# Optimization experiments

Hardware: AMD Instinct MI355X
Metric: run time of the kernel (lower is better)

The kernel has to match this reference:

```python
import jax, jax.numpy as jnp
import numpy as np

NEG = -1e9  # finite stand-in for -inf so downstream grads stay finite
NUM_HEADS = 16


def phm_linear(x, A, S, b):
    # PHM weight: W = sum_i kron(A[i], S[i]) -> (n*kin, n*kout)
    n, kin, kout = S.shape
    W = jnp.einsum('nab,nkl->akbl', A, S).reshape(n * kin, n * kout)
    return x @ W + b


def layer_norm(x, g, b, eps=1e-5):
    mu = jnp.mean(x, axis=-1, keepdims=True)
    var = jnp.var(x, axis=-1, keepdims=True)
    return (x - mu) / jnp.sqrt(var + eps) * g + b


def masking(V, lens):
    # DAG transition mask: vertex i may transition to j>i with j < len[b].
    i = jnp.arange(V)
    tri = i[None, :] > i[:, None]                       # (V,V) j > i
    valid = i[None, None, :] < lens[:, None, None]      # (B,1,V)
    m = tri[None, :, :] & valid
    dead = ~m.any(-1)                                   # (B,V) rows with no valid successor
    eye = jnp.eye(V, dtype=bool)
    m = m | (dead[:, :, None] & eye[None])              # keep softmax finite on dead rows
    return m, dead


def setup_inputs() -> dict:
    key = jax.random.key(0)
    ks = jax.random.split(key, 8)
    B, V, E, VOC = 8, 512, 1024, 32000
    s = 0.02
    return {
        'x': jax.random.normal(ks[0], (B, V, E), jnp.float32),
        'vertex_lens': jax.random.randint(ks[1], (B,), V // 2, V + 1),
        'ln_g': jnp.ones((E,), jnp.float32),
        'ln_b': jnp.zeros((E,), jnp.float32),
        'attn_A': jax.random.normal(ks[2], (4, 4, 4), jnp.float32) * 0.5,
        'attn_S': jax.random.normal(ks[3], (4, 256, 512), jnp.float32) * s,
        'attn_b': jnp.zeros((2 * E,), jnp.float32),
        'gate_A': jax.random.normal(ks[4], (4, 4, 4), jnp.float32) * 0.5,
        'gate_S': jax.random.normal(ks[5], (4, 256, 4), jnp.float32) * s,
        'gate_b': jnp.zeros((NUM_HEADS,), jnp.float32),
        'lm_A': jax.random.normal(ks[6], (2, 2, 2), jnp.float32) * 0.5,
        'lm_S': jax.random.normal(ks[7], (2, 512, 16000), jnp.float32) * s,
        'lm_b': jnp.zeros((VOC,), jnp.float32),
    }


def reference(x, vertex_lens, ln_g, ln_b, attn_A, attn_S, attn_b,
              gate_A, gate_S, gate_b, lm_A, lm_S, lm_b):
    B, V, E = x.shape
    H = NUM_HEADS
    cs = E // H
    xn = layer_norm(x, ln_g, ln_b)
    m, r = masking(V, vertex_lens)
    # gate over heads (B,V,H)
    g = jax.nn.log_softmax(phm_linear(xn, gate_A, gate_S, gate_b), axis=-1)
    qk = phm_linear(xn, attn_A, attn_S, attn_b)
    q, k = jnp.split(qk, 2, axis=-1)
    q = q.reshape(B, V, H, cs)
    k = k.reshape(B, V, H, cs)
    scores = jnp.einsum('bihf,bjhf->bijh', q, k) / jnp.asarray(np.sqrt(cs), jnp.float32)
    scores = jnp.where(m[..., None], scores, NEG)
    scores = jax.nn.log_softmax(scores, axis=2)          # normalize over successors j
    scores = jnp.where(r[:, :, None, None], NEG, scores)  # kill rows past length
    transition_matrix = jax.nn.logsumexp(scores + g[:, :, None, :], axis=-1)  # (B,V,V)
    vocab_log_probs = jax.nn.log_softmax(phm_linear(xn, lm_A, lm_S, lm_b), axis=-1)
    return transition_matrix, vocab_log_probs
```

## Files before the change

### kernel.cpp

```cpp
#include <hip/hip_runtime.h>
#include <hip/hip_bf16.h>
#include <stdint.h>

typedef __bf16 bf16x8 __attribute__((ext_vector_type(8)));
typedef __bf16 bf16x4 __attribute__((ext_vector_type(4)));
typedef float  f32x4  __attribute__((ext_vector_type(4)));

typedef __attribute__((address_space(3))) unsigned int as3_uint;
typedef const __attribute__((address_space(1))) unsigned int as1_uint;

#define NEGC (-1e9f)

__device__ __forceinline__ void async16(void* ldsPtr, const void* gPtr) {
    __builtin_amdgcn_global_load_lds((as1_uint*)(uintptr_t)gPtr,
                                     (as3_uint*)(uintptr_t)ldsPtr, 16, 0, 0);
}

__global__ __launch_bounds__(256) void ln_kernel(const float* __restrict__ x,
                                                 const float* __restrict__ gw,
                                                 const float* __restrict__ bw,
                                                 __bf16* __restrict__ xn) {
    __shared__ float red[8];
    size_t row = blockIdx.x;
    int t = threadIdx.x;
    const float4* xr = (const float4*)(x + row * 1024);
    float4 v = xr[t];
    float s  = v.x + v.y + v.z + v.w;
    float ss = v.x*v.x + v.y*v.y + v.z*v.z + v.w*v.w;
    #pragma unroll
    for (int o = 32; o; o >>= 1) { s += __shfl_xor(s, o); ss += __shfl_xor(ss, o); }
    int wave = t >> 6, lane = t & 63;
    if (lane == 0) { red[wave*2] = s; red[wave*2+1] = ss; }
    __syncthreads();
    float S  = red[0] + red[2] + red[4] + red[6];
    float SS = red[1] + red[3] + red[5] + red[7];
    float mu  = S * (1.0f/1024.0f);
    float var = SS * (1.0f/1024.0f) - mu*mu;
    float rs  = rsqrtf(var + 1e-5f);
    float4 gv = ((const float4*)gw)[t];
    float4 bv = ((const float4*)bw)[t];
    bf16x4 o4;
    o4[0] = (__bf16)((v.x-mu)*rs*gv.x + bv.x);
    o4[1] = (__bf16)((v.y-mu)*rs*gv.y + bv.y);
    o4[2] = (__bf16)((v.z-mu)*rs*gv.z + bv.z);
    o4[3] = (__bf16)((v.w-mu)*rs*gv.w + bv.w);
    ((bf16x4*)(xn + row*1024))[t] = o4;
}

__global__ __launch_bounds__(256) void phm_build(const float* __restrict__ A,
                                                 const float* __restrict__ S,
                                                 __bf16* __restrict__ Wt,
                                                 int nn, int kin, int kout) {
    __shared__ float sh[4][32][65];
    __shared__ float shA[64];
    int t  = threadIdx.x;
    int l0 = blockIdx.x * 64;
    int k0 = blockIdx.y * 32;
    int kt = nn * kin;
    if (t < nn*nn*nn) shA[t] = A[t];
    for (int n = 0; n < nn; ++n) {
        #pragma unroll
        for (int i = 0; i < 8; ++i) {
            int e = t + i*256;
            int kk = e >> 6, ll = e & 63;
            sh[n][kk][ll] = S[((size_t)(n*kin) + k0 + kk)*kout + l0 + ll];
        }
    }
    __syncthreads();
    for (int a = 0; a < nn; ++a)
        for (int b = 0; b < nn; ++b) {
            #pragma unroll
            for (int i = 0; i < 8; ++i) {
                int e = t + i*256;
                int kk = e & 31, ll = e >> 5;
                float val = 0.f;
                for (int n = 0; n < nn; ++n)
                    val += shA[(n*nn + a)*nn + b] * sh[n][kk][ll];
                Wt[(size_t)(b*kout + l0 + ll)*kt + a*kin + k0 + kk] = (__bf16)val;
            }
        }
}

__global__ __launch_bounds__(256) void gatew_kernel(const float* __restrict__ A,
                                                    const float* __restrict__ S,
                                                    float* __restrict__ W) {
    int idx = blockIdx.x*256 + threadIdx.x;
    int r = idx >> 4, c = idx & 15;
    int a = r >> 8, k = r & 255, b = c >> 2, l = c & 3;
    float v = 0.f;
    #pragma unroll
    for (int n = 0; n < 4; ++n)
        v += A[(n*4 + a)*4 + b] * S[((size_t)(n*256 + k))*4 + l];
    W[idx] = v;
}

template<int SWZ, int BF16OUT>
__global__ __launch_bounds__(256) void gemm_bt_t(const __bf16* __restrict__ A,
                                                 const __bf16* __restrict__ Bt,
                                                 const float* __restrict__ bias,
                                                 void* __restrict__ Cv,
                                                 int M, int N, int K) {
    __shared__ __align__(16) __bf16 As[128*64];
    __shared__ __align__(16) __bf16 Bs[128*64];
    int tid  = threadIdx.x;
    int wave = tid >> 6, lane = tid & 63;
    int m0, n0;
    if (SWZ) {
        int bid  = blockIdx.x;
        int wg   = (bid & 7) * 1000 + (bid >> 3);
        int band = wg / 2000;
        int rem  = wg % 2000;
        int nt   = rem >> 3;
        int mt   = band * 8 + (rem & 7);
        m0 = mt * 128; n0 = nt * 128;
    } else {
        m0 = blockIdx.y * 128; n0 = blockIdx.x * 128;
    }
    int wm = (wave >> 1) * 64, wn = (wave & 1) * 64;
    int lrow = lane & 15, lk = lane >> 4;
    f32x4 acc[4][4] = {};
    for (int k0 = 0; k0 < K; k0 += 64) {
        #pragma unroll
        for (int q = 0; q < 4; ++q) {
            int o   = q*4096 + tid*16;
            int row = o >> 7;
            int sp  = (o >> 4) & 7;
            int s   = sp ^ (row & 7);
            async16((char*)As + q*4096 + wave*1024,
                    (const char*)A  + ((size_t)(m0+row)*K + k0 + s*8)*2);
            async16((char*)Bs + q*4096 + wave*1024,
                    (const char*)Bt + ((size_t)(n0+row)*K + k0 + s*8)*2);
        }
        __syncthreads();
        #pragma unroll
        for (int kk = 0; kk < 2; ++kk) {
            bf16x8 af[4], bfr[4];
            #pragma unroll
            for (int mi = 0; mi < 4; ++mi) {
                int r = wm + mi*16 + lrow;
                int off = r*128 + ((kk*64 + lk*16) ^ ((r & 7) << 4));
                af[mi] = *(const bf16x8*)((const char*)As + off);
            }
            #pragma unroll
            for (int ni = 0; ni < 4; ++ni) {
                int r = wn + ni*16 + lrow;
                int off = r*128 + ((kk*64 + lk*16) ^ ((r & 7) << 4));
                bfr[ni] = *(const bf16x8*)((const char*)Bs + off);
            }
            #pragma unroll
            for (int mi = 0; mi < 4; ++mi)
                #pragma unroll
                for (int ni = 0; ni < 4; ++ni)
                    acc[mi][ni] = __builtin_amdgcn_mfma_f32_16x16x32_bf16(
                        af[mi], bfr[ni], acc[mi][ni], 0, 0, 0);
        }
        __syncthreads();
    }
    #pragma unroll
    for (int ni = 0; ni < 4; ++ni) {
        int col = n0 + wn + ni*16 + lrow;
        float bv = bias ? bias[col] : 0.f;
        #pragma unroll
        for (int mi = 0; mi < 4; ++mi) {
            #pragma unroll
            for (int r = 0; r < 4; ++r) {
                int rowg = m0 + wm + mi*16 + lk*4 + r;
                float val = acc[mi][ni][r] + bv;
                if (BF16OUT) {
                    __bf16* rowp = (__bf16*)((char*)Cv + (size_t)rowg*N*4);
                    rowp[col] = (__bf16)val;
                } else {
                    ((float*)Cv)[(size_t)rowg*N + col] = val;
                }
            }
        }
    }
}

__global__ __launch_bounds__(256) void gate_kernel(const __bf16* __restrict__ xn,
                                                   const float* __restrict__ Wg,
                                                   const float* __restrict__ gb,
                                                   float* __restrict__ Gp) {
    __shared__ float xr[16][65];
    __shared__ float red[16][17];
    size_t row = blockIdx.x;
    int t = threadIdx.x;
    bf16x4 v = ((const bf16x4*)(xn + row*1024))[t];
    #pragma unroll
    for (int q = 0; q < 4; ++q) {
        int e = t*4 + q;
        xr[e >> 6][e & 63] = (float)v[q];
    }
    __syncthreads();
    int h = t & 15, sl = t >> 4;
    float p = 0.f;
    #pragma unroll
    for (int u = 0; u < 64; ++u) p += xr[sl][u] * Wg[(sl*64 + u)*16 + h];
    red[sl][h] = p;
    __syncthreads();
    if (t < 16) {
        float logit = gb[t];
        #pragma unroll
        for (int s2 = 0; s2 < 16; ++s2) logit += red[s2][t];
        float m = logit;
        #pragma unroll
        for (int o = 8; o; o >>= 1) m = fmaxf(m, __shfl_xor(m, o, 16));
        float e = __expf(logit - m);
        float ssum = e;
        #pragma unroll
        for (int o = 8; o; o >>= 1) ssum += __shfl_xor(ssum, o, 16);
        Gp[row*16 + t] = e / ssum;
    }
}

__global__ __launch_bounds__(256) void scores_kernel(const float* __restrict__ qk,
                                                     const float* __restrict__ Gp,
                                                     const int* __restrict__ lens,
                                                     float* __restrict__ out) {
    __shared__ float qs[8][1024];
    __shared__ float gps[8][16];
    __shared__ float wredB[2][4][8];
    int bid = blockIdx.x;
    int b   = bid & 7;
    int i0  = (bid >> 3) * 8;
    int t   = threadIdx.x;
    int wave = t >> 6, lane = t & 63;
    int len = lens[b];
    const float4* qbase = (const float4*)(qk + ((size_t)b*512 + i0)*2048);
    #pragma unroll
    for (int s = 0; s < 8; ++s) {
        int e = t + s*256;
        int ti = e >> 8, c4 = e & 255;
        ((float4*)qs)[e] = qbase[ti*512 + c4];
    }
    if (t < 128) gps[t >> 4][t & 15] = Gp[((size_t)b*512 + i0 + (t >> 4))*16 + (t & 15)];
    __syncthreads();
    int j0 = t, j1 = t + 256;
    const float4* kp0 = (const float4*)(qk + ((size_t)b*512 + j0)*2048 + 1024);
    const float4* kp1 = (const float4*)(qk + ((size_t)b*512 + j1)*2048 + 1024);
    float acc0[8] = {}, acc1[8] = {}, mace[8] = {};
    for (int h = 0; h < 16; ++h) {
        float4 kv0[16], kv1[16];
        #pragma unroll
        for (int u = 0; u < 16; ++u) { kv0[u] = kp0[h*16 + u]; kv1[u] = kp1[h*16 + u]; }
        float pex0[8], pex1[8];
        #pragma unroll
        for (int ti = 0; ti < 8; ++ti) {
            const float* qrow = &qs[ti][h*64];
            float d0 = 0.f, d1 = 0.f;
            #pragma unroll
            for (int u = 0; u < 16; ++u) {
                float q0 = qrow[u*4+0], q1 = qrow[u*4+1], q2 = qrow[u*4+2], q3 = qrow[u*4+3];
                d0 += kv0[u].x*q0 + kv0[u].y*q1 + kv0[u].z*q2 + kv0[u].w*q3;
                d1 += kv1[u].x*q0 + kv1[u].y*q1 + kv1[u].z*q2 + kv1[u].w*q3;
            }
            int i = i0 + ti;
            float sc0 = (j0 > i && j0 < len) ? d0 * 0.125f : NEGC;
            float sc1 = (j1 > i && j1 < len) ? d1 * 0.125f : NEGC;
            float pe0 = __expf(sc0), pe1 = __expf(sc1);
            pex0[ti] = pe0; pex1[ti] = pe1;
            float vv = pe0 + pe1;
            #pragma unroll
            for (int o = 32; o; o >>= 1) vv += __shfl_xor(vv, o);
            if (lane == 0) wredB[h & 1][wave][ti] = vv;
        }
        __syncthreads();
        #pragma unroll
        for (int ti = 0; ti < 8; ++ti) {
            float gs = wredB[h & 1][0][ti] + wredB[h & 1][1][ti]
                     + wredB[h & 1][2][ti] + wredB[h & 1][3][ti];
            float inv = 1.0f / gs;
            float g = gps[ti][h];
            acc0[ti] += pex0[ti] * inv * g;
            acc1[ti] += pex1[ti] * inv * g;
            mace[ti] += g * inv;
        }
    }
    #pragma unroll
    for (int ti = 0; ti < 8; ++ti) {
        int i = i0 + ti;
        float lm = NEGC + __logf(mace[ti]);
        float v0, v1;
        if (i >= len - 1) { v0 = NEGC; v1 = NEGC; }
        else {
            v0 = (j0 > i && j0 < len) ? __logf(acc0[ti]) : lm;
            v1 = (j1 > i && j1 < len) ? __logf(acc1[ti]) : lm;
        }
        out[((size_t)b*512 + i)*512 + j0] = v0;
        out[((size_t)b*512 + i)*512 + j1] = v1;
    }
}

__global__ __launch_bounds__(256) void vocab_softmax_bf16(float* __restrict__ out) {
    __shared__ __align__(16) __bf16 srow[32000];
    __shared__ float red[8];
    size_t row = blockIdx.x;
    char* rowbase = (char*)out + row * (size_t)32000 * 4;
    const bf16x8* g8 = (const bf16x8*)rowbase;
    bf16x8* s8 = (bf16x8*)srow;
    int t = threadIdx.x, wave = t >> 6, lane = t & 63;
    float mx = -1e30f;
    for (int v = t; v < 4000; v += 256) {
        bf16x8 c = g8[v];
        s8[v] = c;
        #pragma unroll
        for (int jj = 0; jj < 8; ++jj) mx = fmaxf(mx, (float)c[jj]);
    }
    #pragma unroll
    for (int o = 32; o; o >>= 1) mx = fmaxf(mx, __shfl_xor(mx, o));
    if (lane == 0) red[wave] = mx;
    __syncthreads();
    mx = fmaxf(fmaxf(red[0], red[1]), fmaxf(red[2], red[3]));
    float sum = 0.f;
    for (int v = t; v < 4000; v += 256) {
        bf16x8 c = s8[v];
        #pragma unroll
        for (int jj = 0; jj < 8; ++jj) sum += __expf((float)c[jj] - mx);
    }
    #pragma unroll
    for (int o = 32; o; o >>= 1) sum += __shfl_xor(sum, o);
    if (lane == 0) red[4 + wave] = sum;
    __syncthreads();
    float lse = mx + __logf(red[4] + red[5] + red[6] + red[7]);
    float4* o4 = (float4*)rowbase;
    for (int u = t; u < 8000; u += 256) {
        bf16x4 c = *(const bf16x4*)(srow + u*4);
        float4 a;
        a.x = (float)c[0] - lse; a.y = (float)c[1] - lse;
        a.z = (float)c[2] - lse; a.w = (float)c[3] - lse;
        o4[u] = a;
    }
}

extern "C" void kernel_launch(void* const* d_in, const int* in_sizes, int n_in,
                              void* d_out, int out_size, void* d_ws, size_t ws_size,
                              hipStream_t stream) {
    (void)in_sizes; (void)n_in; (void)out_size; (void)ws_size;
    const float* x      = (const float*)d_in[0];
    const int*   lens   = (const int*)  d_in[1];
    const float* ln_g   = (const float*)d_in[2];
    const float* ln_b   = (const float*)d_in[3];
    const float* attn_A = (const float*)d_in[4];
    const float* attn_S = (const float*)d_in[5];
    const float* attn_b = (const float*)d_in[6];
    const float* gate_A = (const float*)d_in[7];
    const float* gate_S = (const float*)d_in[8];
    const float* gate_b = (const float*)d_in[9];
    const float* lm_A   = (const float*)d_in[10];
    const float* lm_S   = (const float*)d_in[11];
    const float* lm_b   = (const float*)d_in[12];

    float* out_trans = (float*)d_out;
    float* out_vocab = out_trans + (size_t)8*512*512;

    char* ws = (char*)d_ws;
    __bf16* xn     = (__bf16*)(ws);
    __bf16* WtAttn = (__bf16*)(ws + 8388608);
    __bf16* WtLm   = (__bf16*)(ws + 12582912);
    float*  Wg     = (float*) (ws + 78118912);
    float*  qkbuf  = (float*) (ws + 78184448);
    float*  Gp     = (float*) (ws + 111738880);

    hipLaunchKernelGGL(ln_kernel,    dim3(4096),     dim3(256), 0, stream, x, ln_g, ln_b, xn);
    hipLaunchKernelGGL(gatew_kernel, dim3(64),       dim3(256), 0, stream, gate_A, gate_S, Wg);
    hipLaunchKernelGGL(phm_build,    dim3(8, 8),     dim3(256), 0, stream, attn_A, attn_S, WtAttn, 4, 256, 512);
    hipLaunchKernelGGL(phm_build,    dim3(250, 16),  dim3(256), 0, stream, lm_A, lm_S, WtLm, 2, 512, 16000);
    hipLaunchKernelGGL((gemm_bt_t<0,0>), dim3(16, 32), dim3(256), 0, stream,
                       xn, WtAttn, attn_b, (void*)qkbuf, 4096, 2048, 1024);
    hipLaunchKernelGGL(gate_kernel,  dim3(4096),     dim3(256), 0, stream, xn, Wg, gate_b, Gp);
    hipLaunchKernelGGL(scores_kernel,dim3(512),      dim3(256), 0, stream, qkbuf, Gp, lens, out_trans);
    hipLaunchKernelGGL((gemm_bt_t<1,1>), dim3(8000),  dim3(256), 0, stream,
                       xn, WtLm, lm_b, (void*)out_vocab, 4096, 32000, 1024);
    hipLaunchKernelGGL(vocab_softmax_bf16, dim3(4096), dim3(256), 0, stream, out_vocab);
}
```

Baseline: 837.3 us.

## Run LM-head GEMM in FP8 e4m3 with MFMA scale instructions

LayerNorm now also writes an FP8 e4m3 copy of the normalized activations, and the LM PHM weight is built directly in FP8, pre-scaled by 16 to keep small weights out of the subnormal range. A new GEMM kernel uses the 16x16x128 f8f6f4 scaled MFMA with K-tiles of 128 and undoes the scale in the epilogue. The goal is to halve operand bandwidth and raise matrix throughput for the largest GEMM, at the cost of much lower precision in the vocab logits. The attention GEMM stays in bf16 and the workspace layout is reorganized.

```diff
diff --git a/kernel.cpp b/kernel.cpp
--- a/kernel.cpp
+++ b/kernel.cpp
@@ -1,10 +1,13 @@
 #include <hip/hip_runtime.h>
 #include <hip/hip_bf16.h>
+#include <hip/hip_fp8.h>
 #include <stdint.h>
 
 typedef __bf16 bf16x8 __attribute__((ext_vector_type(8)));
 typedef __bf16 bf16x4 __attribute__((ext_vector_type(4)));
 typedef float  f32x4  __attribute__((ext_vector_type(4)));
+typedef int    i32x4  __attribute__((ext_vector_type(4)));
+typedef int    i32x8  __attribute__((ext_vector_type(8)));
 
 typedef __attribute__((address_space(3))) unsigned int as3_uint;
 typedef const __attribute__((address_space(1))) unsigned int as1_uint;
@@ -19,7 +22,8 @@
 __global__ __launch_bounds__(256) void ln_kernel(const float* __restrict__ x,
                                                  const float* __restrict__ gw,
                                                  const float* __restrict__ bw,
-                                                 __bf16* __restrict__ xn) {
+                                                 __bf16* __restrict__ xn,
+                                                 unsigned char* __restrict__ xn8) {
     __shared__ float red[8];
     size_t row = blockIdx.x;
     int t = threadIdx.x;
@@ -39,17 +43,24 @@
     float rs  = rsqrtf(var + 1e-5f);
     float4 gv = ((const float4*)gw)[t];
     float4 bv = ((const float4*)bw)[t];
+    float f0 = (v.x-mu)*rs*gv.x + bv.x;
+    float f1 = (v.y-mu)*rs*gv.y + bv.y;
+    float f2 = (v.z-mu)*rs*gv.z + bv.z;
+    float f3 = (v.w-mu)*rs*gv.w + bv.w;
     bf16x4 o4;
-    o4[0] = (__bf16)((v.x-mu)*rs*gv.x + bv.x);
-    o4[1] = (__bf16)((v.y-mu)*rs*gv.y + bv.y);
-    o4[2] = (__bf16)((v.z-mu)*rs*gv.z + bv.z);
-    o4[3] = (__bf16)((v.w-mu)*rs*gv.w + bv.w);
+    o4[0] = (__bf16)f0; o4[1] = (__bf16)f1; o4[2] = (__bf16)f2; o4[3] = (__bf16)f3;
     ((bf16x4*)(xn + row*1024))[t] = o4;
-}
-
+    unsigned int pk = (unsigned)__hip_fp8_e4m3(f0).__x
+                    | ((unsigned)__hip_fp8_e4m3(f1).__x << 8)
+                    | ((unsigned)__hip_fp8_e4m3(f2).__x << 16)
+                    | ((unsigned)__hip_fp8_e4m3(f3).__x << 24);
+    ((unsigned int*)(xn8 + row*1024))[t] = pk;
+}
+
+template<int OUT>
 __global__ __launch_bounds__(256) void phm_build(const float* __restrict__ A,
                                                  const float* __restrict__ S,
-                                                 __bf16* __restrict__ Wt,
+                                                 void* __restrict__ Wt,
                                                  int nn, int kin, int kout) {
     __shared__ float sh[4][32][65];
     __shared__ float shA[64];
@@ -76,7 +87,9 @@
                 float val = 0.f;
                 for (int n = 0; n < nn; ++n)
                     val += shA[(n*nn + a)*nn + b] * sh[n][kk][ll];
-                Wt[(size_t)(b*kout + l0 + ll)*kt + a*kin + k0 + kk] = (__bf16)val;
+                size_t idx = (size_t)(b*kout + l0 + ll)*kt + a*kin + k0 + kk;
+                if (OUT == 0) ((__bf16*)Wt)[idx] = (__bf16)val;
+                else          ((unsigned char*)Wt)[idx] = __hip_fp8_e4m3(val * 16.0f).__x;
             }
         }
 }
@@ -94,28 +107,16 @@
     W[idx] = v;
 }
 
-template<int SWZ, int BF16OUT>
-__global__ __launch_bounds__(256) void gemm_bt_t(const __bf16* __restrict__ A,
-                                                 const __bf16* __restrict__ Bt,
-                                                 const float* __restrict__ bias,
-                                                 void* __restrict__ Cv,
-                                                 int M, int N, int K) {
+__global__ __launch_bounds__(256) void gemm_bt(const __bf16* __restrict__ A,
+                                               const __bf16* __restrict__ Bt,
+                                               const float* __restrict__ bias,
+                                               float* __restrict__ C,
+                                               int M, int N, int K) {
     __shared__ __align__(16) __bf16 As[128*64];
     __shared__ __align__(16) __bf16 Bs[128*64];
     int tid  = threadIdx.x;
     int wave = tid >> 6, lane = tid & 63;
-    int m0, n0;
-    if (SWZ) {
-        int bid  = blockIdx.x;
-        int wg   = (bid & 7) * 1000 + (bid >> 3);
-        int band = wg / 2000;
-        int rem  = wg % 2000;
-        int nt   = rem >> 3;
-        int mt   = band * 8 + (rem & 7);
-        m0 = mt * 128; n0 = nt * 128;
-    } else {
-        m0 = blockIdx.y * 128; n0 = blockIdx.x * 128;
-    }
+    int m0 = blockIdx.y * 128, n0 = blockIdx.x * 128;
     int wm = (wave >> 1) * 64, wn = (wave & 1) * 64;
     int lrow = lane & 15, lk = lane >> 4;
     f32x4 acc[4][4] = {};
@@ -165,13 +166,81 @@
             #pragma unroll
             for (int r = 0; r < 4; ++r) {
                 int rowg = m0 + wm + mi*16 + lk*4 + r;
-                float val = acc[mi][ni][r] + bv;
-                if (BF16OUT) {
-                    __bf16* rowp = (__bf16*)((char*)Cv + (size_t)rowg*N*4);
-                    rowp[col] = (__bf16)val;
-                } else {
-                    ((float*)Cv)[(size_t)rowg*N + col] = val;
-                }
+                C[(size_t)rowg*N + col] = acc[mi][ni][r] + bv;
+            }
+        }
+    }
+}
+
+__global__ __launch_bounds__(256) void gemm_mx_lm(const unsigned char* __restrict__ A8,
+                                                  const unsigned char* __restrict__ B8,
+                                                  const float* __restrict__ bias,
+                                                  void* __restrict__ Cv) {
+    const int K = 1024, N = 32000;
+    __shared__ __align__(16) unsigned char As[128*128];
+    __shared__ __align__(16) unsigned char Bs[128*128];
+    int tid = threadIdx.x;
+    int wave = tid >> 6, lane = tid & 63;
+    int bid  = blockIdx.x;
+    int wg   = (bid & 7) * 1000 + (bid >> 3);
+    int band = wg / 2000;
+    int rem  = wg % 2000;
+    int nt   = rem >> 3;
+    int mt   = band * 8 + (rem & 7);
+    int m0 = mt * 128, n0 = nt * 128;
+    int wm = (wave >> 1) * 64, wn = (wave & 1) * 64;
+    int lrow = lane & 15, lk = lane >> 4;
+    f32x4 acc[4][4] = {};
+    for (int k0 = 0; k0 < K; k0 += 128) {
+        #pragma unroll
+        for (int q = 0; q < 4; ++q) {
+            int o = q*4096 + tid*16;
+            int r = o >> 7;
+            int p = (o >> 4) & 7;
+            int g = p ^ (r & 7);
+            async16((char*)As + q*4096 + wave*1024,
+                    (const char*)A8 + (size_t)(m0+r)*K + k0 + g*16);
+            async16((char*)Bs + q*4096 + wave*1024,
+                    (const char*)B8 + (size_t)(n0+r)*K + k0 + g*16);
+        }
+        __syncthreads();
+        i32x8 af[4], bfr[4];
+        #pragma unroll
+        for (int mi = 0; mi < 4; ++mi) {
+            int r = wm + mi*16 + lrow;
+            int c0 = lk*2;
+            i32x4 lo = *(const i32x4*)(As + r*128 + ((c0    ^ (r&7))*16));
+            i32x4 hi = *(const i32x4*)(As + r*128 + (((c0+1) ^ (r&7))*16));
+            af[mi] = __builtin_shufflevector(lo, hi, 0,1,2,3,4,5,6,7);
+        }
+        #pragma unroll
+        for (int ni = 0; ni < 4; ++ni) {
+            int r = wn + ni*16 + lrow;
+            int c0 = lk*2;
+            i32x4 lo = *(const i32x4*)(Bs + r*128 + ((c0    ^ (r&7))*16));
+            i32x4 hi = *(const i32x4*)(Bs + r*128 + (((c0+1) ^ (r&7))*16));
+            bfr[ni] = __builtin_shufflevector(lo, hi, 0,1,2,3,4,5,6,7);
+        }
+        #pragma unroll
+        for (int mi = 0; mi < 4; ++mi)
+            #pragma unroll
+            for (int ni = 0; ni < 4; ++ni)
+                acc[mi][ni] = __builtin_amdgcn_mfma_scale_f32_16x16x128_f8f6f4(
+                    af[mi], bfr[ni], acc[mi][ni],
+                    0 , 0 , 0, 127, 0, 127);
+        __syncthreads();
+    }
+    #pragma unroll
+    for (int ni = 0; ni < 4; ++ni) {
+        int col = n0 + wn + ni*16 + lrow;
+        float bv = bias ? bias[col] : 0.f;
+        #pragma unroll
+        for (int mi = 0; mi < 4; ++mi) {
+            #pragma unroll
+            for (int r = 0; r < 4; ++r) {
+                int rowg = m0 + wm + mi*16 + lk*4 + r;
+                float val = acc[mi][ni][r] * 0.0625f + bv;
+                ((__bf16*)((char*)Cv + (size_t)rowg * N * 4))[col] = (__bf16)val;
             }
         }
     }
@@ -354,22 +423,23 @@
     float* out_vocab = out_trans + (size_t)8*512*512;
 
     char* ws = (char*)d_ws;
-    __bf16* xn     = (__bf16*)(ws);
-    __bf16* WtAttn = (__bf16*)(ws + 8388608);
-    __bf16* WtLm   = (__bf16*)(ws + 12582912);
-    float*  Wg     = (float*) (ws + 78118912);
-    float*  qkbuf  = (float*) (ws + 78184448);
-    float*  Gp     = (float*) (ws + 111738880);
-
-    hipLaunchKernelGGL(ln_kernel,    dim3(4096),     dim3(256), 0, stream, x, ln_g, ln_b, xn);
+    __bf16*        xn     = (__bf16*)(ws);
+    unsigned char* xn8    = (unsigned char*)(ws + 8388608);
+    __bf16*        WtAttn = (__bf16*)(ws + 12582912);
+    unsigned char* WtLm8  = (unsigned char*)(ws + 16777216);
+    float*         Wg     = (float*)(ws + 49545216);
+    float*         qkbuf  = (float*)(ws + 49610752);
+    float*         Gp     = (float*)(ws + 83165184);
+
+    hipLaunchKernelGGL(ln_kernel,    dim3(4096),     dim3(256), 0, stream, x, ln_g, ln_b, xn, xn8);
     hipLaunchKernelGGL(gatew_kernel, dim3(64),       dim3(256), 0, stream, gate_A, gate_S, Wg);
-    hipLaunchKernelGGL(phm_build,    dim3(8, 8),     dim3(256), 0, stream, attn_A, attn_S, WtAttn, 4, 256, 512);
-    hipLaunchKernelGGL(phm_build,    dim3(250, 16),  dim3(256), 0, stream, lm_A, lm_S, WtLm, 2, 512, 16000);
-    hipLaunchKernelGGL((gemm_bt_t<0,0>), dim3(16, 32), dim3(256), 0, stream,
-                       xn, WtAttn, attn_b, (void*)qkbuf, 4096, 2048, 1024);
+    hipLaunchKernelGGL((phm_build<0>), dim3(8, 8),   dim3(256), 0, stream, attn_A, attn_S, (void*)WtAttn, 4, 256, 512);
+    hipLaunchKernelGGL((phm_build<1>), dim3(250, 16),dim3(256), 0, stream, lm_A, lm_S, (void*)WtLm8, 2, 512, 16000);
+    hipLaunchKernelGGL(gemm_bt,      dim3(16, 32),   dim3(256), 0, stream,
+                       xn, WtAttn, attn_b, qkbuf, 4096, 2048, 1024);
     hipLaunchKernelGGL(gate_kernel,  dim3(4096),     dim3(256), 0, stream, xn, Wg, gate_b, Gp);
     hipLaunchKernelGGL(scores_kernel,dim3(512),      dim3(256), 0, stream, qkbuf, Gp, lens, out_trans);
-    hipLaunchKernelGGL((gemm_bt_t<1,1>), dim3(8000),  dim3(256), 0, stream,
-                       xn, WtLm, lm_b, (void*)out_vocab, 4096, 32000, 1024);
+    hipLaunchKernelGGL(gemm_mx_lm,   dim3(8000),     dim3(256), 0, stream,
+                       xn8, WtLm8, lm_b, (void*)out_vocab);
     hipLaunchKernelGGL(vocab_softmax_bf16, dim3(4096), dim3(256), 0, stream, out_vocab);
 }
```

Result: faster. 725.7 us (-13.3%).
